# Kernel optimization log

Measured on AMD Instinct MI355X. Metric: run time of the kernel, lower is better.

Reference implementation:

```python
import jax, jax.numpy as jnp
import numpy as np

N_NODES = 50000
N_EDGES = 800000
D = 256
N_LAYERS = 2


def setup_inputs() -> dict:
    key = jax.random.key(0)
    k1, k2, k3, k4, k5, k6 = jax.random.split(key, 6)
    inp = {}
    inp["input"] = jax.random.normal(k1, (N_NODES, D), dtype=jnp.float32)
    inp["edge_index"] = jax.random.randint(k2, (2, N_EDGES), 0, N_NODES, dtype=jnp.int64)
    # learned params: initial dense projection + per-conv GCN weights
    scale = 1.0 / np.sqrt(D)
    inp["weight"] = jax.random.normal(k3, (D, D), dtype=jnp.float32) * scale
    inp["bias"] = jnp.zeros((D,), dtype=jnp.float32)
    inp["conv_w"] = jax.random.normal(k4, (N_LAYERS, D, D), dtype=jnp.float32) * scale
    inp["conv_b"] = jnp.zeros((N_LAYERS, D), dtype=jnp.float32)
    return inp


def _gcn_conv(x, W, b, src, dst, n):
    # Standard GCNConv: x' = D^{-1/2} (A + I) D^{-1/2} (x W) + b
    h = x @ W  # [N, D]
    loops = jnp.arange(n, dtype=src.dtype)
    s = jnp.concatenate([src, loops])
    d = jnp.concatenate([dst, loops])
    deg = jax.ops.segment_sum(jnp.ones(s.shape[0], dtype=x.dtype), d, num_segments=n)
    dinv = jnp.where(deg > 0, deg ** -0.5, 0.0)
    norm = dinv[s] * dinv[d]  # [E+N]
    msg = h[s] * norm[:, None]  # gather + scale  [E+N, D]
    return jax.ops.segment_sum(msg, d, num_segments=n) + b  # scatter-add


def reference(input, edge_index, weight, bias, conv_w, conv_b):
    n = input.shape[0]
    src, dst = edge_index[0], edge_index[1]
    # dropout=0 / eval mode -> identity
    x = jax.nn.relu(input @ weight + bias)
    for i in range(conv_w.shape[0]):
        x = jax.nn.relu(_gcn_conv(x, conv_w[i], conv_b[i], src, dst, n))
    return x
```

## Files before the change

### kernel.cpp

```cpp
#include <hip/hip_runtime.h>

#define D 256
typedef unsigned short u16;
typedef __attribute__((ext_vector_type(8))) short bf16x8;
typedef __attribute__((ext_vector_type(4))) float f32x4;

__device__ __forceinline__ float bf2f(u16 u) {
    union { unsigned int i; float f; } x; x.i = ((unsigned int)u) << 16; return x.f;
}
__device__ __forceinline__ u16 f2bf(float f) {
    union { float f; unsigned int i; } x; x.f = f;
    unsigned int r = x.i + 0x7fff + ((x.i >> 16) & 1);
    return (u16)(r >> 16);
}
__device__ __forceinline__ unsigned int cvtpk_bf16(float lo, float hi) {
    unsigned int r;
    asm("v_cvt_pk_bf16_f32 %0, %1, %2" : "=v"(r) : "v"(lo), "v"(hi));
    return r;
}
__device__ __forceinline__ void gload16(const void* g, void* l) {
    __builtin_amdgcn_global_load_lds(
        (const __attribute__((address_space(1))) void*)g,
        (__attribute__((address_space(3))) void*)l, 16, 0, 0);
}
__device__ __forceinline__ bf16x8 gload_row(const u16* p) {
    bf16x8 r;
    asm volatile("global_load_dwordx4 %0, %1, off" : "=&v"(r) : "v"(p));
    return r;
}


__global__ void init_kernel(int* __restrict__ deg, int* __restrict__ cursor, int n) {
    int i = blockIdx.x * blockDim.x + threadIdx.x;
    if (i < n) { deg[i] = 1; cursor[i] = 0; }
}

__global__ void hist_kernel(const int* __restrict__ dst, int* __restrict__ deg, int e) {
    int i = blockIdx.x * blockDim.x + threadIdx.x;
    int b = i * 4;
    if (b + 3 < e) {
        int4 v = *reinterpret_cast<const int4*>(&dst[b]);
        atomicAdd(&deg[v.x], 1); atomicAdd(&deg[v.y], 1);
        atomicAdd(&deg[v.z], 1); atomicAdd(&deg[v.w], 1);
    } else {
        for (int j = b; j < e; ++j) atomicAdd(&deg[dst[j]], 1);
    }
}


__global__ __launch_bounds__(256) void scan_phase1(
    const int* __restrict__ deg, int* __restrict__ bsum,
    float* __restrict__ dinv, int n) {
    __shared__ int red[256];
    int t = threadIdx.x;
    int i0 = blockIdx.x * 1024 + t * 4;
    int s = 0;
    if (i0 + 3 < n) {
        int4 v = *reinterpret_cast<const int4*>(&deg[i0]);
        s = v.x + v.y + v.z + v.w - 4;
        float4 dv;
        dv.x = rsqrtf((float)v.x); dv.y = rsqrtf((float)v.y);
        dv.z = rsqrtf((float)v.z); dv.w = rsqrtf((float)v.w);
        *reinterpret_cast<float4*>(&dinv[i0]) = dv;
    } else {
        for (int j = i0; j < n && j < i0 + 4; ++j) {
            s += deg[j] - 1;
            dinv[j] = rsqrtf((float)deg[j]);
        }
    }
    red[t] = s;
    __syncthreads();
    for (int off = 128; off > 0; off >>= 1) {
        if (t < off) red[t] += red[t + off];
        __syncthreads();
    }
    if (t == 0) bsum[blockIdx.x] = red[0];
}

__global__ __launch_bounds__(256) void scan_phase2(
    const int* __restrict__ bsum, int* __restrict__ boff,
    int* __restrict__ rowptr, int nblk, int n) {
    __shared__ int sums[256];
    int t = threadIdx.x;
    int v = (t < nblk) ? bsum[t] : 0;
    int orig = v;
    sums[t] = v;
    __syncthreads();
    for (int off = 1; off < 256; off <<= 1) {
        int u = (t >= off) ? sums[t - off] : 0;
        __syncthreads();
        sums[t] += u;
        __syncthreads();
    }
    if (t < nblk) boff[t] = sums[t] - orig;
    if (t == nblk - 1) rowptr[n] = sums[t];
}

__global__ __launch_bounds__(256) void scan_phase3(
    const int* __restrict__ deg, const int* __restrict__ boff,
    int* __restrict__ rowptr, int n) {
    __shared__ int sums[256];
    int t = threadIdx.x;
    int i0 = blockIdx.x * 1024 + t * 4;
    int d0 = 0, d1 = 0, d2 = 0, d3 = 0;
    if (i0 + 3 < n) {
        int4 v = *reinterpret_cast<const int4*>(&deg[i0]);
        d0 = v.x - 1; d1 = v.y - 1; d2 = v.z - 1; d3 = v.w - 1;
    } else {
        if (i0 + 0 < n) d0 = deg[i0 + 0] - 1;
        if (i0 + 1 < n) d1 = deg[i0 + 1] - 1;
        if (i0 + 2 < n) d2 = deg[i0 + 2] - 1;
        if (i0 + 3 < n) d3 = deg[i0 + 3] - 1;
    }
    int ts = d0 + d1 + d2 + d3;
    sums[t] = ts;
    __syncthreads();
    for (int off = 1; off < 256; off <<= 1) {
        int u = (t >= off) ? sums[t - off] : 0;
        __syncthreads();
        sums[t] += u;
        __syncthreads();
    }
    int pre = boff[blockIdx.x] + sums[t] - ts;
    if (i0 + 0 < n) rowptr[i0 + 0] = pre; pre += d0;
    if (i0 + 1 < n) rowptr[i0 + 1] = pre; pre += d1;
    if (i0 + 2 < n) rowptr[i0 + 2] = pre; pre += d2;
    if (i0 + 3 < n) rowptr[i0 + 3] = pre;
}

__global__ void fill_kernel(const int* __restrict__ src, const int* __restrict__ dst,
                            const int* __restrict__ rowptr, int* __restrict__ cursor,
                            int* __restrict__ csr, int e) {
    int i = blockIdx.x * blockDim.x + threadIdx.x;
    int b = i * 4;
    if (b + 3 < e) {
        int4 s4 = *reinterpret_cast<const int4*>(&src[b]);
        int4 d4 = *reinterpret_cast<const int4*>(&dst[b]);
        int p;
        p = atomicAdd(&cursor[d4.x], 1); csr[rowptr[d4.x] + p] = s4.x;
        p = atomicAdd(&cursor[d4.y], 1); csr[rowptr[d4.y] + p] = s4.y;
        p = atomicAdd(&cursor[d4.z], 1); csr[rowptr[d4.z] + p] = s4.z;
        p = atomicAdd(&cursor[d4.w], 1); csr[rowptr[d4.w] + p] = s4.w;
    } else {
        for (int j = b; j < e; ++j) {
            int d = dst[j];
            int p = atomicAdd(&cursor[d], 1);
            csr[rowptr[d] + p] = src[j];
        }
    }
}


__global__ __launch_bounds__(256) void transpose_cvt_kernel(
    const float* __restrict__ W, u16* __restrict__ Wt) {
    __shared__ float t[32][33];
    int bx = blockIdx.x * 32, by = blockIdx.y * 32;
    int tx = threadIdx.x & 31, ty = threadIdx.x >> 5;
#pragma unroll
    for (int i = 0; i < 32; i += 8)
        t[ty + i][tx] = W[(size_t)(bx + ty + i) * D + by + tx];
    __syncthreads();
#pragma unroll
    for (int i = 0; i < 32; i += 8)
        Wt[(size_t)(by + ty + i) * D + bx + tx] = f2bf(t[tx][ty + i]);
}


__global__ __launch_bounds__(256) void mfma_gemm(
    const u16* __restrict__ A, const u16* __restrict__ Bt,
    const float* __restrict__ dinv,
    u16* __restrict__ C, int M)
{
    __shared__ u16 As[128 * 32];
    __shared__ u16 Bs[128 * 32];
    const int tid = threadIdx.x;
    const int lane = tid & 63;
    const int wave = tid >> 6;
    const int wr = wave >> 1, wc = wave & 1;
    const int row0 = blockIdx.y * 128, col0 = blockIdx.x * 128;
    const int l16 = lane & 15, kg = lane >> 4;

    f32x4 acc[4][4] = {};

    for (int k0 = 0; k0 < D; k0 += 32) {
#pragma unroll
        for (int i = 0; i < 2; ++i) {
            int idx = i * 256 + tid;
            int r = idx >> 2, c = idx & 3;
            int csw = c ^ ((r >> 1) & 3);
            char* ldsbase_a = (char*)As + ((i * 256 + (tid & ~63)) << 4);
            char* ldsbase_b = (char*)Bs + ((i * 256 + (tid & ~63)) << 4);
            int grow = row0 + r; if (grow >= M) grow = M - 1;
            gload16(&A[(size_t)grow * D + k0 + csw * 8], ldsbase_a);
            gload16(&Bt[(size_t)(col0 + r) * D + k0 + csw * 8], ldsbase_b);
        }
        __syncthreads();
        bf16x8 af[4], bfr[4];
        int ksw = kg ^ ((l16 >> 1) & 3);
#pragma unroll
        for (int m = 0; m < 4; ++m)
            af[m] = *reinterpret_cast<const bf16x8*>(&As[(wr * 64 + m * 16 + l16) * 32 + ksw * 8]);
#pragma unroll
        for (int nn = 0; nn < 4; ++nn)
            bfr[nn] = *reinterpret_cast<const bf16x8*>(&Bs[(wc * 64 + nn * 16 + l16) * 32 + ksw * 8]);
#pragma unroll
        for (int m = 0; m < 4; ++m)
#pragma unroll
            for (int nn = 0; nn < 4; ++nn)
                acc[m][nn] = __builtin_amdgcn_mfma_f32_16x16x32_bf16(
                    af[m], bfr[nn], acc[m][nn], 0, 0, 0);
        __syncthreads();
    }

#pragma unroll
    for (int m = 0; m < 4; ++m) {
#pragma unroll
        for (int nn = 0; nn < 4; ++nn) {
            int gcol = col0 + wc * 64 + nn * 16 + l16;
#pragma unroll
            for (int j = 0; j < 4; ++j) {
                int grow = row0 + wr * 64 + m * 16 + kg * 4 + j;
                if (grow >= M) continue;
                C[(size_t)grow * D + gcol] = f2bf(acc[m][nn][j] * dinv[grow]);
            }
        }
    }
}

__global__ __launch_bounds__(256) void mfma_gemm_f32a(
    const float* __restrict__ A, const u16* __restrict__ Bt,
    const float* __restrict__ bias,
    u16* __restrict__ C, int M)
{
    __shared__ u16 As[128 * 32];
    __shared__ u16 Bs[128 * 32];
    const int tid = threadIdx.x;
    const int lane = tid & 63;
    const int wave = tid >> 6;
    const int wr = wave >> 1, wc = wave & 1;
    const int row0 = blockIdx.y * 128, col0 = blockIdx.x * 128;
    const int l16 = lane & 15, kg = lane >> 4;

    f32x4 acc[4][4] = {};

    for (int k0 = 0; k0 < D; k0 += 32) {
#pragma unroll
        for (int i = 0; i < 2; ++i) {
            int idx = i * 256 + tid;
            int r = idx >> 2, c = idx & 3;
            int csw = c ^ ((r >> 1) & 3);
            char* ldsbase_b = (char*)Bs + ((i * 256 + (tid & ~63)) << 4);
            gload16(&Bt[(size_t)(col0 + r) * D + k0 + csw * 8], ldsbase_b);
        }
#pragma unroll
        for (int i = 0; i < 2; ++i) {
            int idx = i * 256 + tid;
            int r = idx >> 2, c = idx & 3;
            int csw = c ^ ((r >> 1) & 3);
            int grow = row0 + r; if (grow >= M) grow = M - 1;
            const float* gp = &A[(size_t)grow * D + k0 + csw * 8];
            float4 v0 = *reinterpret_cast<const float4*>(gp);
            float4 v1 = *reinterpret_cast<const float4*>(gp + 4);
            uint4 w;
            w.x = cvtpk_bf16(v0.x, v0.y);
            w.y = cvtpk_bf16(v0.z, v0.w);
            w.z = cvtpk_bf16(v1.x, v1.y);
            w.w = cvtpk_bf16(v1.z, v1.w);
            *reinterpret_cast<uint4*>((char*)As + (idx << 4)) = w;
        }
        __syncthreads();
        bf16x8 af[4], bfr[4];
        int ksw = kg ^ ((l16 >> 1) & 3);
#pragma unroll
        for (int m = 0; m < 4; ++m)
            af[m] = *reinterpret_cast<const bf16x8*>(&As[(wr * 64 + m * 16 + l16) * 32 + ksw * 8]);
#pragma unroll
        for (int nn = 0; nn < 4; ++nn)
            bfr[nn] = *reinterpret_cast<const bf16x8*>(&Bs[(wc * 64 + nn * 16 + l16) * 32 + ksw * 8]);
#pragma unroll
        for (int m = 0; m < 4; ++m)
#pragma unroll
            for (int nn = 0; nn < 4; ++nn)
                acc[m][nn] = __builtin_amdgcn_mfma_f32_16x16x32_bf16(
                    af[m], bfr[nn], acc[m][nn], 0, 0, 0);
        __syncthreads();
    }

#pragma unroll
    for (int m = 0; m < 4; ++m) {
#pragma unroll
        for (int nn = 0; nn < 4; ++nn) {
            int gcol = col0 + wc * 64 + nn * 16 + l16;
#pragma unroll
            for (int j = 0; j < 4; ++j) {
                int grow = row0 + wr * 64 + m * 16 + kg * 4 + j;
                if (grow >= M) continue;
                C[(size_t)grow * D + gcol] = f2bf(fmaxf(acc[m][nn][j] + bias[gcol], 0.f));
            }
        }
    }
}

__global__ __launch_bounds__(256) void agg_kernel(
    const u16* __restrict__ hn, const int* __restrict__ rowptr,
    const int* __restrict__ csr, const float* __restrict__ dinv,
    const float* __restrict__ bias,
    u16* __restrict__ out_bf, float* __restrict__ out_f32, int n)
{
    int wave = threadIdx.x >> 6;
    int lane = threadIdx.x & 63;
    int node = blockIdx.x * 4 + wave;
    if (node >= n) return;
    int h = lane >> 5;
    int l5 = lane & 31;
    int c8 = l5 * 8;

    float a[8] = {0.f, 0.f, 0.f, 0.f, 0.f, 0.f, 0.f, 0.f};

#define ACC8(vv) { \
    a[0] += bf2f((u16)(vv)[0]); a[1] += bf2f((u16)(vv)[1]); \
    a[2] += bf2f((u16)(vv)[2]); a[3] += bf2f((u16)(vv)[3]); \
    a[4] += bf2f((u16)(vv)[4]); a[5] += bf2f((u16)(vv)[5]); \
    a[6] += bf2f((u16)(vv)[6]); a[7] += bf2f((u16)(vv)[7]); }
#define ROWP(s) (&hn[(size_t)(s) * D + c8])

    if (h == 0) {
        bf16x8 v = *reinterpret_cast<const bf16x8*>(ROWP(node));
        ACC8(v);
    }

    int e0 = rowptr[node], e1 = rowptr[node + 1];
    for (int base = e0; base < e1; base += 64) {
        int bi = base + lane;
        int idx = (bi < e1) ? csr[bi] : 0;
        int cnt = e1 - base; if (cnt > 64) cnt = 64;
        int it = 0;
        for (; it + 16 <= cnt; it += 16) {
            int s0 = __shfl(idx, it + 0  + h);
            int s1 = __shfl(idx, it + 2  + h);
            int s2 = __shfl(idx, it + 4  + h);
            int s3 = __shfl(idx, it + 6  + h);
            int s4 = __shfl(idx, it + 8  + h);
            int s5 = __shfl(idx, it + 10 + h);
            int s6 = __shfl(idx, it + 12 + h);
            int s7 = __shfl(idx, it + 14 + h);
            bf16x8 v0 = gload_row(ROWP(s0));
            bf16x8 v1 = gload_row(ROWP(s1));
            bf16x8 v2 = gload_row(ROWP(s2));
            bf16x8 v3 = gload_row(ROWP(s3));
            bf16x8 v4 = gload_row(ROWP(s4));
            bf16x8 v5 = gload_row(ROWP(s5));
            bf16x8 v6 = gload_row(ROWP(s6));
            bf16x8 v7 = gload_row(ROWP(s7));
            asm volatile("s_waitcnt vmcnt(0)" ::: "memory");
            __builtin_amdgcn_sched_barrier(0);
            ACC8(v0); ACC8(v1); ACC8(v2); ACC8(v3);
            ACC8(v4); ACC8(v5); ACC8(v6); ACC8(v7);
        }
        for (; it + 8 <= cnt; it += 8) {
            int s0 = __shfl(idx, it + 0 + h);
            int s1 = __shfl(idx, it + 2 + h);
            int s2 = __shfl(idx, it + 4 + h);
            int s3 = __shfl(idx, it + 6 + h);
            bf16x8 v0 = gload_row(ROWP(s0));
            bf16x8 v1 = gload_row(ROWP(s1));
            bf16x8 v2 = gload_row(ROWP(s2));
            bf16x8 v3 = gload_row(ROWP(s3));
            asm volatile("s_waitcnt vmcnt(0)" ::: "memory");
            __builtin_amdgcn_sched_barrier(0);
            ACC8(v0); ACC8(v1); ACC8(v2); ACC8(v3);
        }
        for (; it + 2 <= cnt; it += 2) {
            int s0 = __shfl(idx, it + h);
            bf16x8 v0 = *reinterpret_cast<const bf16x8*>(ROWP(s0));
            ACC8(v0);
        }
        if (it < cnt) {
            int s0 = __shfl(idx, it);
            if (h == 0) {
                bf16x8 v0 = *reinterpret_cast<const bf16x8*>(ROWP(s0));
                ACC8(v0);
            }
        }
    }
#undef ACC8
#undef ROWP

#pragma unroll
    for (int j = 0; j < 8; ++j) a[j] += __shfl(a[j], lane ^ 32);

    if (h == 0) {
        float di = dinv[node];
#pragma unroll
        for (int j = 0; j < 8; ++j) a[j] = fmaxf(a[j] * di + bias[c8 + j], 0.f);
        if (out_bf) {
            bf16x8 o;
#pragma unroll
            for (int j = 0; j < 8; ++j) o[j] = (short)f2bf(a[j]);
            *reinterpret_cast<bf16x8*>(&out_bf[(size_t)node * D + c8]) = o;
        } else {
            float4 o0, o1;
            o0.x = a[0]; o0.y = a[1]; o0.z = a[2]; o0.w = a[3];
            o1.x = a[4]; o1.y = a[5]; o1.z = a[6]; o1.w = a[7];
            *reinterpret_cast<float4*>(&out_f32[(size_t)node * D + c8 + 0]) = o0;
            *reinterpret_cast<float4*>(&out_f32[(size_t)node * D + c8 + 4]) = o1;
        }
    }
}


extern "C" void kernel_launch(void* const* d_in, const int* in_sizes, int n_in,
                              void* d_out, int out_size, void* d_ws, size_t ws_size,
                              hipStream_t stream) {
    const float* input  = (const float*)d_in[0];
    const int*   edge   = (const int*)d_in[1];
    const float* weight = (const float*)d_in[2];
    const float* bias   = (const float*)d_in[3];
    const float* conv_w = (const float*)d_in[4];
    const float* conv_b = (const float*)d_in[5];
    float* out = (float*)d_out;

    const int n = in_sizes[0] / D;
    const int E = in_sizes[1] / 2;
    const int* src = edge;
    const int* dst = edge + E;

    char* ws = (char*)d_ws;
    size_t off = 0;
    auto alloc = [&](size_t bytes) -> void* {
        void* p = ws + off;
        off = (off + bytes + 255) & ~(size_t)255;
        return p;
    };
    u16*   bufA   = (u16*)alloc((size_t)n * D * sizeof(u16));
    u16*   bufB   = (u16*)alloc((size_t)n * D * sizeof(u16));
    u16*   Wt     = (u16*)alloc((size_t)3 * D * D * sizeof(u16));
    int*   deg    = (int*)alloc((size_t)n * sizeof(int));
    int*   cursor = (int*)alloc((size_t)n * sizeof(int));
    float* dinv   = (float*)alloc((size_t)n * sizeof(float));
    int*   rowptr = (int*)alloc((size_t)(n + 1) * sizeof(int));
    int*   csr    = (int*)alloc((size_t)E * sizeof(int));
    int    nscan  = (n + 1023) / 1024;
    int*   bsum   = (int*)alloc((size_t)nscan * sizeof(int));
    int*   boff   = (int*)alloc((size_t)nscan * sizeof(int));

    int nb = (n + 255) / 256;
    int eb4 = (E / 4 + 255) / 256;
    init_kernel<<<nb, 256, 0, stream>>>(deg, cursor, n);
    hist_kernel<<<eb4, 256, 0, stream>>>(dst, deg, E);
    scan_phase1<<<nscan, 256, 0, stream>>>(deg, bsum, dinv, n);
    scan_phase2<<<1, 256, 0, stream>>>(bsum, boff, rowptr, nscan, n);
    scan_phase3<<<nscan, 256, 0, stream>>>(deg, boff, rowptr, n);
    fill_kernel<<<eb4, 256, 0, stream>>>(src, dst, rowptr, cursor, csr, E);

    dim3 tgrid(8, 8);
    transpose_cvt_kernel<<<tgrid, 256, 0, stream>>>(weight, Wt);
    transpose_cvt_kernel<<<tgrid, 256, 0, stream>>>(conv_w, Wt + D * D);
    transpose_cvt_kernel<<<tgrid, 256, 0, stream>>>(conv_w + D * D, Wt + 2 * D * D);

    dim3 ggrid(D / 128, (n + 127) / 128);
    mfma_gemm_f32a<<<ggrid, 256, 0, stream>>>(input, Wt, bias, bufA, n);
    mfma_gemm<<<ggrid, 256, 0, stream>>>(bufA, Wt + D * D, dinv, bufB, n);
    agg_kernel<<<(n + 3) / 4, 256, 0, stream>>>(bufB, rowptr, csr, dinv, conv_b, bufA, nullptr, n);
    mfma_gemm<<<ggrid, 256, 0, stream>>>(bufA, Wt + 2 * D * D, dinv, bufB, n);
    agg_kernel<<<(n + 3) / 4, 256, 0, stream>>>(bufB, rowptr, csr, dinv, conv_b + D, nullptr, out, n);
}
```

Baseline: 329.2 us.

## Split aggregation into two column-half passes to shrink gather working set

The aggregation kernel now processes only 128 of the 256 feature columns per launch, with each lane loading 4 bf16 values (8 bytes) instead of 8. It is launched twice per layer on the two column halves. The aim is to halve the footprint of the randomly gathered rows so that each pass's working set (about 12.8 MB of bf16) fits better in L2/MALL, improving hit rates for the irregular gathers. In exchange, CSR indices and rowptr are read twice, launch count grows, and each load is narrower, which adds per-edge index and shuffle overhead.

```diff
diff --git a/kernel.cpp b/kernel.cpp
--- a/kernel.cpp
+++ b/kernel.cpp
@@ -3,6 +3,7 @@
 #define D 256
 typedef unsigned short u16;
 typedef __attribute__((ext_vector_type(8))) short bf16x8;
+typedef __attribute__((ext_vector_type(4))) unsigned short u16x4;
 typedef __attribute__((ext_vector_type(4))) float f32x4;
 
 __device__ __forceinline__ float bf2f(u16 u) {
@@ -23,9 +24,9 @@
         (const __attribute__((address_space(1))) void*)g,
         (__attribute__((address_space(3))) void*)l, 16, 0, 0);
 }
-__device__ __forceinline__ bf16x8 gload_row(const u16* p) {
-    bf16x8 r;
-    asm volatile("global_load_dwordx4 %0, %1, off" : "=&v"(r) : "v"(p));
+__device__ __forceinline__ u16x4 gload_half(const u16* p) {
+    u16x4 r;
+    asm volatile("global_load_dwordx2 %0, %1, off" : "=&v"(r) : "v"(p));
     return r;
 }
 
@@ -313,20 +314,18 @@
     if (node >= n) return;
     int h = lane >> 5;
     int l5 = lane & 31;
-    int c8 = l5 * 8;
-
-    float a[8] = {0.f, 0.f, 0.f, 0.f, 0.f, 0.f, 0.f, 0.f};
-
-#define ACC8(vv) { \
-    a[0] += bf2f((u16)(vv)[0]); a[1] += bf2f((u16)(vv)[1]); \
-    a[2] += bf2f((u16)(vv)[2]); a[3] += bf2f((u16)(vv)[3]); \
-    a[4] += bf2f((u16)(vv)[4]); a[5] += bf2f((u16)(vv)[5]); \
-    a[6] += bf2f((u16)(vv)[6]); a[7] += bf2f((u16)(vv)[7]); }
-#define ROWP(s) (&hn[(size_t)(s) * D + c8])
+    int c4 = l5 * 4;
+
+    float a[4] = {0.f, 0.f, 0.f, 0.f};
+
+#define ACC4(vv) { \
+    a[0] += bf2f((vv)[0]); a[1] += bf2f((vv)[1]); \
+    a[2] += bf2f((vv)[2]); a[3] += bf2f((vv)[3]); }
+#define ROWP(s) (&hn[(size_t)(s) * D + c4])
 
     if (h == 0) {
-        bf16x8 v = *reinterpret_cast<const bf16x8*>(ROWP(node));
-        ACC8(v);
+        u16x4 v = *reinterpret_cast<const u16x4*>(ROWP(node));
+        ACC4(v);
     }
 
     int e0 = rowptr[node], e1 = rowptr[node + 1];
@@ -344,66 +343,64 @@
             int s5 = __shfl(idx, it + 10 + h);
             int s6 = __shfl(idx, it + 12 + h);
             int s7 = __shfl(idx, it + 14 + h);
-            bf16x8 v0 = gload_row(ROWP(s0));
-            bf16x8 v1 = gload_row(ROWP(s1));
-            bf16x8 v2 = gload_row(ROWP(s2));
-            bf16x8 v3 = gload_row(ROWP(s3));
-            bf16x8 v4 = gload_row(ROWP(s4));
-            bf16x8 v5 = gload_row(ROWP(s5));
-            bf16x8 v6 = gload_row(ROWP(s6));
-            bf16x8 v7 = gload_row(ROWP(s7));
+            u16x4 v0 = gload_half(ROWP(s0));
+            u16x4 v1 = gload_half(ROWP(s1));
+            u16x4 v2 = gload_half(ROWP(s2));
+            u16x4 v3 = gload_half(ROWP(s3));
+            u16x4 v4 = gload_half(ROWP(s4));
+            u16x4 v5 = gload_half(ROWP(s5));
+            u16x4 v6 = gload_half(ROWP(s6));
+            u16x4 v7 = gload_half(ROWP(s7));
             asm volatile("s_waitcnt vmcnt(0)" ::: "memory");
             __builtin_amdgcn_sched_barrier(0);
-            ACC8(v0); ACC8(v1); ACC8(v2); ACC8(v3);
-            ACC8(v4); ACC8(v5); ACC8(v6); ACC8(v7);
+            ACC4(v0); ACC4(v1); ACC4(v2); ACC4(v3);
+            ACC4(v4); ACC4(v5); ACC4(v6); ACC4(v7);
         }
         for (; it + 8 <= cnt; it += 8) {
             int s0 = __shfl(idx, it + 0 + h);
             int s1 = __shfl(idx, it + 2 + h);
             int s2 = __shfl(idx, it + 4 + h);
             int s3 = __shfl(idx, it + 6 + h);
-            bf16x8 v0 = gload_row(ROWP(s0));
-            bf16x8 v1 = gload_row(ROWP(s1));
-            bf16x8 v2 = gload_row(ROWP(s2));
-            bf16x8 v3 = gload_row(ROWP(s3));
+            u16x4 v0 = gload_half(ROWP(s0));
+            u16x4 v1 = gload_half(ROWP(s1));
+            u16x4 v2 = gload_half(ROWP(s2));
+            u16x4 v3 = gload_half(ROWP(s3));
             asm volatile("s_waitcnt vmcnt(0)" ::: "memory");
             __builtin_amdgcn_sched_barrier(0);
-            ACC8(v0); ACC8(v1); ACC8(v2); ACC8(v3);
+            ACC4(v0); ACC4(v1); ACC4(v2); ACC4(v3);
         }
         for (; it + 2 <= cnt; it += 2) {
             int s0 = __shfl(idx, it + h);
-            bf16x8 v0 = *reinterpret_cast<const bf16x8*>(ROWP(s0));
-            ACC8(v0);
+            u16x4 v0 = *reinterpret_cast<const u16x4*>(ROWP(s0));
+            ACC4(v0);
         }
         if (it < cnt) {
             int s0 = __shfl(idx, it);
             if (h == 0) {
-                bf16x8 v0 = *reinterpret_cast<const bf16x8*>(ROWP(s0));
-                ACC8(v0);
+                u16x4 v0 = *reinterpret_cast<const u16x4*>(ROWP(s0));
+                ACC4(v0);
             }
         }
     }
-#undef ACC8
+#undef ACC4
 #undef ROWP
 
 #pragma unroll
-    for (int j = 0; j < 8; ++j) a[j] += __shfl(a[j], lane ^ 32);
+    for (int j = 0; j < 4; ++j) a[j] += __shfl(a[j], lane ^ 32);
 
     if (h == 0) {
         float di = dinv[node];
 #pragma unroll
-        for (int j = 0; j < 8; ++j) a[j] = fmaxf(a[j] * di + bias[c8 + j], 0.f);
+        for (int j = 0; j < 4; ++j) a[j] = fmaxf(a[j] * di + bias[c4 + j], 0.f);
         if (out_bf) {
-            bf16x8 o;
-#pragma unroll
-            for (int j = 0; j < 8; ++j) o[j] = (short)f2bf(a[j]);
-            *reinterpret_cast<bf16x8*>(&out_bf[(size_t)node * D + c8]) = o;
+            u16x4 o;
+#pragma unroll
+            for (int j = 0; j < 4; ++j) o[j] = f2bf(a[j]);
+            *reinterpret_cast<u16x4*>(&out_bf[(size_t)node * D + c4]) = o;
         } else {
-            float4 o0, o1;
-            o0.x = a[0]; o0.y = a[1]; o0.z = a[2]; o0.w = a[3];
-            o1.x = a[4]; o1.y = a[5]; o1.z = a[6]; o1.w = a[7];
-            *reinterpret_cast<float4*>(&out_f32[(size_t)node * D + c8 + 0]) = o0;
-            *reinterpret_cast<float4*>(&out_f32[(size_t)node * D + c8 + 4]) = o1;
+            float4 o;
+            o.x = a[0]; o.y = a[1]; o.z = a[2]; o.w = a[3];
+            *reinterpret_cast<float4*>(&out_f32[(size_t)node * D + c4]) = o;
         }
     }
 }
@@ -459,9 +456,13 @@
     transpose_cvt_kernel<<<tgrid, 256, 0, stream>>>(conv_w + D * D, Wt + 2 * D * D);
 
     dim3 ggrid(D / 128, (n + 127) / 128);
+    dim3 agrid((n + 3) / 4);
+
     mfma_gemm_f32a<<<ggrid, 256, 0, stream>>>(input, Wt, bias, bufA, n);
     mfma_gemm<<<ggrid, 256, 0, stream>>>(bufA, Wt + D * D, dinv, bufB, n);
-    agg_kernel<<<(n + 3) / 4, 256, 0, stream>>>(bufB, rowptr, csr, dinv, conv_b, bufA, nullptr, n);
+    agg_kernel<<<agrid, 256, 0, stream>>>(bufB,       rowptr, csr, dinv, conv_b,       bufA,       nullptr, n);
+    agg_kernel<<<agrid, 256, 0, stream>>>(bufB + 128, rowptr, csr, dinv, conv_b + 128, bufA + 128, nullptr, n);
     mfma_gemm<<<ggrid, 256, 0, stream>>>(bufA, Wt + 2 * D * D, dinv, bufB, n);
-    agg_kernel<<<(n + 3) / 4, 256, 0, stream>>>(bufB, rowptr, csr, dinv, conv_b + D, nullptr, out, n);
-}
+    agg_kernel<<<agrid, 256, 0, stream>>>(bufB,       rowptr, csr, dinv, conv_b + D,       nullptr, out,       n);
+    agg_kernel<<<agrid, 256, 0, stream>>>(bufB + 128, rowptr, csr, dinv, conv_b + D + 128, nullptr, out + 128, n);
+}
```

Result: slower. 338.8 us (+2.9%).
